# Optimization experiments

Measured on AMD Instinct MI355X. Metric: run time of the kernel, lower is better.

## Reference

```python
import jax, jax.numpy as jnp
import numpy as np

N = 50000      # nodes
E = 800000     # edges (before self-loops)
H = 4          # heads
C = 64         # hidden_unit per head
IN = 256       # input_dim
OUT = 64       # output_dim
NEG = 0.2      # LeakyReLU slope in GATConv
EPS = 1e-5     # BatchNorm eps


def setup_inputs() -> dict:
    key = jax.random.key(0)
    ks = jax.random.split(key, 12)
    s = 0.05
    HC = H * C
    return {
        'x': jax.random.normal(ks[0], (N, IN), dtype=jnp.float32),
        'edge_index': jax.random.randint(ks[1], (2, E), 0, N, dtype=jnp.int64),
        # GATConv layer 1
        'W1': jax.random.normal(ks[2], (IN, HC), dtype=jnp.float32) * s,
        'att_src1': jax.random.normal(ks[3], (H, C), dtype=jnp.float32) * s,
        'att_dst1': jax.random.normal(ks[4], (H, C), dtype=jnp.float32) * s,
        'b1': jnp.zeros((HC,), jnp.float32),
        # GATConv layer 2
        'W2': jax.random.normal(ks[5], (HC, HC), dtype=jnp.float32) * s,
        'att_src2': jax.random.normal(ks[6], (H, C), dtype=jnp.float32) * s,
        'att_dst2': jax.random.normal(ks[7], (H, C), dtype=jnp.float32) * s,
        'b2': jnp.zeros((HC,), jnp.float32),
        # BatchNorms
        'g1': jnp.ones((HC,), jnp.float32), 'beta1': jnp.zeros((HC,), jnp.float32),
        'g2': jnp.ones((HC,), jnp.float32), 'beta2': jnp.zeros((HC,), jnp.float32),
        # final Linear
        'Wl': jax.random.normal(ks[8], (HC, OUT), dtype=jnp.float32) * s,
        'bl': jnp.zeros((OUT,), jnp.float32),
    }


def gat_layer(x, src, dst, W, a_src, a_dst, b):
    # x: [N, F_in] -> per-head features [N, H, C]
    xh = (x @ W).reshape(-1, H, C)
    alpha_src = jnp.einsum('nhc,hc->nh', xh, a_src)   # [N, H]
    alpha_dst = jnp.einsum('nhc,hc->nh', xh, a_dst)   # [N, H]
    e = jax.nn.leaky_relu(alpha_src[src] + alpha_dst[dst], NEG)  # [Etot, H]
    # segment softmax over edges grouped by destination node
    m = jax.ops.segment_max(e, dst, num_segments=N)              # [N, H]
    ex = jnp.exp(e - m[dst])
    den = jax.ops.segment_sum(ex, dst, num_segments=N)           # [N, H]
    alpha = ex / (den[dst] + 1e-16)                              # [Etot, H]
    # weighted scatter-add aggregation
    out = jax.ops.segment_sum(alpha[:, :, None] * xh[src], dst, num_segments=N)
    return out.reshape(-1, H * C) + b


def batchnorm(x, g, beta):
    mu = x.mean(axis=0)
    var = x.var(axis=0)
    return (x - mu) * jax.lax.rsqrt(var + EPS) * g + beta


def reference(x, edge_index, W1, att_src1, att_dst1, b1,
              W2, att_src2, att_dst2, b2, g1, beta1, g2, beta2, Wl, bl):
    # GATConv adds self-loops by default
    loops = jnp.arange(N, dtype=edge_index.dtype)
    src = jnp.concatenate([edge_index[0], loops])
    dst = jnp.concatenate([edge_index[1], loops])
    h = batchnorm(gat_layer(x, src, dst, W1, att_src1, att_dst1, b1), g1, beta1)
    # dropout is identity in eval mode
    h = batchnorm(gat_layer(h, src, dst, W2, att_src2, att_dst2, b2), g2, beta2)
    emb = h @ Wl + bl
    out = jax.nn.log_softmax(emb, axis=1)
    return (out, emb)
```

## Files before the change

### kernel.cpp

```cpp
#include <hip/hip_runtime.h>
#include <cstdint>

#define NNODES 50000
#define NEDGES 800000
#define ETOT   (NEDGES + NNODES)
#define HEADS 4
#define CH 64
#define HC 256
#define INDIM 256
#define OUTDIM 64
#define NEG_SLOPE 0.2f
#define BN_EPS 1e-5f
#define NB 128

typedef unsigned short u16;
typedef __attribute__((ext_vector_type(8))) short short8;
typedef __attribute__((ext_vector_type(8))) unsigned short ushort8v;
typedef __attribute__((ext_vector_type(4))) float floatx4;

__device__ inline float bf2f(u16 u) {
    union { unsigned int i; float f; } c;
    c.i = ((unsigned int)u) << 16;
    return c.f;
}
__device__ inline u16 f2bf(float f) {
    union { float f; unsigned int i; } c;
    c.f = f;
    unsigned int u = c.i + 0x7fff + ((c.i >> 16) & 1);
    return (u16)(u >> 16);
}
__device__ inline void async16(u16* lds, const u16* g) {
    __builtin_amdgcn_global_load_lds(
        (const __attribute__((address_space(1))) unsigned int*)g,
        (__attribute__((address_space(3))) unsigned int*)lds,
        16, 0, 0);
}


__global__ void hist_kernel(const int* __restrict__ ei, int* __restrict__ cnt) {
    int t = blockIdx.x * blockDim.x + threadIdx.x;
    if (t >= ETOT) return;
    int d = (t < NEDGES) ? ei[NEDGES + t] : (t - NEDGES);
    atomicAdd(&cnt[d], 1);
}

__global__ void scan1_kernel(const int* __restrict__ cnt, int* __restrict__ row_off,
                             int* __restrict__ blockSums) {
    __shared__ int tsum[256];
    const int tid = threadIdx.x;
    const int base = blockIdx.x * 4096 + tid * 16;
    int local[16];
    int run = 0;
#pragma unroll
    for (int i = 0; i < 16; ++i) {
        int idx = base + i;
        int v = (idx < NNODES) ? cnt[idx] : 0;
        local[i] = run;
        run += v;
    }
    tsum[tid] = run;
    __syncthreads();
    for (int d = 1; d < 256; d <<= 1) {
        int v = (tid >= d) ? tsum[tid - d] : 0;
        __syncthreads();
        tsum[tid] += v;
        __syncthreads();
    }
    int excl = (tid == 0) ? 0 : tsum[tid - 1];
#pragma unroll
    for (int i = 0; i < 16; ++i) {
        int idx = base + i;
        if (idx < NNODES) row_off[idx] = excl + local[i];
    }
    if (tid == 0) blockSums[blockIdx.x] = tsum[255];
}

__global__ void scan2_kernel(int* __restrict__ row_off, const int* __restrict__ blockSums,
                             int* __restrict__ nxt) {
    __shared__ int sprefix;
    if (threadIdx.x == 0) {
        int p = 0;
        for (int b = 0; b < (int)blockIdx.x; ++b) p += blockSums[b];
        sprefix = p;
    }
    __syncthreads();
    int prefix = sprefix;
    int base = blockIdx.x * 4096 + threadIdx.x * 16;
#pragma unroll
    for (int i = 0; i < 16; ++i) {
        int idx = base + i;
        if (idx < NNODES) {
            int v = row_off[idx] + prefix;
            row_off[idx] = v;
            nxt[idx] = v;
        }
    }
    if (blockIdx.x == 0 && threadIdx.x == 0) row_off[NNODES] = ETOT;
}

__global__ void fill_csr_kernel(const int* __restrict__ ei, int* __restrict__ nxt,
                                int* __restrict__ csr_src, int* __restrict__ csr_dst) {
    int t = blockIdx.x * blockDim.x + threadIdx.x;
    if (t >= ETOT) return;
    int s, d;
    if (t < NEDGES) { s = ei[t]; d = ei[NEDGES + t]; }
    else            { s = d = t - NEDGES; }
    int pos = atomicAdd(&nxt[d], 1);
    csr_src[pos] = s;
    csr_dst[pos] = d;
}


__global__ void castx_kernel(const float* __restrict__ x, u16* __restrict__ xb, int n4) {
    int t = blockIdx.x * blockDim.x + threadIdx.x;
    if (t >= n4) return;
    float4 v = *(const float4*)&x[(size_t)t * 4];
    ushort4 o;
    o.x = f2bf(v.x); o.y = f2bf(v.y); o.z = f2bf(v.z); o.w = f2bf(v.w);
    *(ushort4*)&xb[(size_t)t * 4] = o;
}

__global__ void wcast_kernel(const float* __restrict__ W, u16* __restrict__ Wt,
                             int K, int Ncols) {
    int t = blockIdx.x * blockDim.x + threadIdx.x;
    if (t >= K * Ncols) return;
    int k = t / Ncols, n = t - k * Ncols;
    Wt[n * K + k] = f2bf(W[t]);
}


__global__ __launch_bounds__(256)
void gemm_bf16_kernel(const u16* __restrict__ A, const u16* __restrict__ Bt,
                      u16* __restrict__ Cbf, const float* __restrict__ bias,
                      int M, int Ncols, int K) {
    __shared__ u16 As[128 * 32];
    __shared__ u16 Bs[128 * 32];
    const int tid = threadIdx.x;
    const int wave = tid >> 6, lane = tid & 63;
    const int q15 = lane & 15, quad = lane >> 4;
    const int rowBase = blockIdx.y * 128;
    const int colBase = blockIdx.x * 128;
    const int waveM = (wave >> 1) * 64, waveN = (wave & 1) * 64;

    floatx4 acc[4][4];
    floatx4 zero = {0.f, 0.f, 0.f, 0.f};
#pragma unroll
    for (int i = 0; i < 4; ++i)
#pragma unroll
        for (int j = 0; j < 4; ++j) acc[i][j] = zero;

    for (int kt = 0; kt < K; kt += 32) {
#pragma unroll
        for (int q = 0; q < 2; ++q) {
            int e8 = (wave * 2 + q) * 64 + lane;
            int r = e8 >> 2;
            int c = (e8 & 3) * 8;
            int ar = rowBase + r; if (ar >= M) ar = M - 1;
            async16(&As[(wave * 2 + q) * 512], &A[(size_t)ar * K + kt + c]);
            int br = colBase + r; if (br >= Ncols) br = Ncols - 1;
            async16(&Bs[(wave * 2 + q) * 512], &Bt[(size_t)br * K + kt + c]);
        }
        __syncthreads();

        short8 af[4], bfr[4];
#pragma unroll
        for (int i = 0; i < 4; ++i)
            af[i] = *(const short8*)&As[(waveM + i * 16 + q15) * 32 + quad * 8];
#pragma unroll
        for (int j = 0; j < 4; ++j)
            bfr[j] = *(const short8*)&Bs[(waveN + j * 16 + q15) * 32 + quad * 8];
#pragma unroll
        for (int i = 0; i < 4; ++i)
#pragma unroll
            for (int j = 0; j < 4; ++j)
                acc[i][j] = __builtin_amdgcn_mfma_f32_16x16x32_bf16(af[i], bfr[j], acc[i][j], 0, 0, 0);
        __syncthreads();
    }

#pragma unroll
    for (int i = 0; i < 4; ++i) {
#pragma unroll
        for (int j = 0; j < 4; ++j) {
            int gcol = colBase + waveN + j * 16 + q15;
            if (gcol >= Ncols) continue;
            float bv = bias ? bias[gcol] : 0.f;
#pragma unroll
            for (int r = 0; r < 4; ++r) {
                int grow = rowBase + waveM + i * 16 + quad * 4 + r;
                if (grow >= M) continue;
                Cbf[(size_t)grow * Ncols + gcol] = f2bf(acc[i][j][r] + bv);
            }
        }
    }
}


__global__ void alpha_kernel(const u16* __restrict__ xh,
                             const float* __restrict__ att_src,
                             const float* __restrict__ att_dst,
                             float* __restrict__ as_, float* __restrict__ ad_) {
    int t = blockIdx.x * blockDim.x + threadIdx.x;
    if (t >= NNODES * HEADS) return;
    int n = t >> 2, h = t & 3;
    const u16* xp = xh + (size_t)n * HC + h * CH;
    const float* sp = att_src + h * CH;
    const float* dp = att_dst + h * CH;
    float s = 0.f, d = 0.f;
#pragma unroll
    for (int c = 0; c < CH; c += 8) {
        ushort8v xv = *(const ushort8v*)&xp[c];
#pragma unroll
        for (int i = 0; i < 8; ++i) {
            float v = bf2f(xv[i]);
            s += v * sp[c + i];
            d += v * dp[c + i];
        }
    }
    as_[t] = s;
    ad_[t] = d;
}


__global__ void wedge_kernel(const int* __restrict__ csr_src, const int* __restrict__ csr_dst,
                             const float* __restrict__ asrc, const float* __restrict__ adst,
                             float* __restrict__ w4) {
    int e = blockIdx.x * blockDim.x + threadIdx.x;
    if (e >= ETOT) return;
    int s = csr_src[e], d = csr_dst[e];
    float4 a = *(const float4*)&asrc[s * 4];
    float4 b = *(const float4*)&adst[d * 4];
    float4 r;
    float v;
    v = a.x + b.x; v = v > 0.f ? v : NEG_SLOPE * v; r.x = __expf(v);
    v = a.y + b.y; v = v > 0.f ? v : NEG_SLOPE * v; r.y = __expf(v);
    v = a.z + b.z; v = v > 0.f ? v : NEG_SLOPE * v; r.z = __expf(v);
    v = a.w + b.w; v = v > 0.f ? v : NEG_SLOPE * v; r.w = __expf(v);
    *(float4*)&w4[(size_t)e * 4] = r;
}


__global__ __launch_bounds__(256)
void aggregate_kernel(const int* __restrict__ row_off, const int* __restrict__ csr_src,
                      const float* __restrict__ w4, const u16* __restrict__ xh,
                      const float* __restrict__ bias, u16* __restrict__ out) {
    const int g = threadIdx.x >> 6;
    const int lane = threadIdx.x & 63;
    const int d = blockIdx.x * 4 + g;
    const int h = lane >> 4;
    const int cbase = lane * 4;
    const int start = row_off[d], end = row_off[d + 1];
    float a0 = 0.f, a1 = 0.f, a2 = 0.f, a3 = 0.f, den = 0.f;
    int e = start;
    for (; e + 3 < end; e += 4) {
        int s0 = csr_src[e], s1 = csr_src[e + 1], s2 = csr_src[e + 2], s3 = csr_src[e + 3];
        float w0 = w4[(size_t)e * 4 + h];
        float w1 = w4[(size_t)(e + 1) * 4 + h];
        float w2 = w4[(size_t)(e + 2) * 4 + h];
        float w3 = w4[(size_t)(e + 3) * 4 + h];
        ushort4 x0 = *(const ushort4*)&xh[(size_t)s0 * HC + cbase];
        ushort4 x1 = *(const ushort4*)&xh[(size_t)s1 * HC + cbase];
        ushort4 x2 = *(const ushort4*)&xh[(size_t)s2 * HC + cbase];
        ushort4 x3 = *(const ushort4*)&xh[(size_t)s3 * HC + cbase];
        den += (w0 + w1) + (w2 + w3);
        a0 += w0 * bf2f(x0.x) + w1 * bf2f(x1.x) + w2 * bf2f(x2.x) + w3 * bf2f(x3.x);
        a1 += w0 * bf2f(x0.y) + w1 * bf2f(x1.y) + w2 * bf2f(x2.y) + w3 * bf2f(x3.y);
        a2 += w0 * bf2f(x0.z) + w1 * bf2f(x1.z) + w2 * bf2f(x2.z) + w3 * bf2f(x3.z);
        a3 += w0 * bf2f(x0.w) + w1 * bf2f(x1.w) + w2 * bf2f(x2.w) + w3 * bf2f(x3.w);
    }
    for (; e < end; ++e) {
        int s0 = csr_src[e];
        float w0 = w4[(size_t)e * 4 + h];
        ushort4 x0 = *(const ushort4*)&xh[(size_t)s0 * HC + cbase];
        den += w0;
        a0 += w0 * bf2f(x0.x);
        a1 += w0 * bf2f(x0.y);
        a2 += w0 * bf2f(x0.z);
        a3 += w0 * bf2f(x0.w);
    }
    float inv = 1.f / (den + 1e-16f);
    ushort4 o;
    o.x = f2bf(a0 * inv + bias[cbase + 0]);
    o.y = f2bf(a1 * inv + bias[cbase + 1]);
    o.z = f2bf(a2 * inv + bias[cbase + 2]);
    o.w = f2bf(a3 * inv + bias[cbase + 3]);
    *(ushort4*)&out[(size_t)d * HC + cbase] = o;
}


__global__ __launch_bounds__(256)
void bn_stats_kernel(const u16* __restrict__ x, float* __restrict__ part) {
    const int tid = threadIdx.x;
    float s[8] = {}, s2[8] = {};
    const size_t total = (size_t)NNODES * HC;
    const size_t stride = (size_t)NB * 256 * 8;
    for (size_t f = ((size_t)blockIdx.x * 256 + tid) * 8; f < total; f += stride) {
        ushort8v v = *(const ushort8v*)&x[f];
#pragma unroll
        for (int i = 0; i < 8; ++i) {
            float t = bf2f(v[i]);
            s[i] += t;
            s2[i] += t * t;
        }
    }
#pragma unroll
    for (int i = 0; i < 8; ++i) {
        s[i] += __shfl_xor(s[i], 32, 64);
        s2[i] += __shfl_xor(s2[i], 32, 64);
    }
    __shared__ float red[4][512];
    const int wave = tid >> 6, lane = tid & 63;
    if (lane < 32) {
#pragma unroll
        for (int i = 0; i < 8; ++i) {
            red[wave][lane * 8 + i] = s[i];
            red[wave][256 + lane * 8 + i] = s2[i];
        }
    }
    __syncthreads();
    for (int j = tid; j < 512; j += 256)
        part[(size_t)blockIdx.x * 512 + j] = red[0][j] + red[1][j] + red[2][j] + red[3][j];
}


__global__ __launch_bounds__(256)
void fold_kernel(const float* __restrict__ W, const float* __restrict__ part,
                 const float* __restrict__ g, const float* __restrict__ beta,
                 const float* __restrict__ baseBias,
                 u16* __restrict__ Wt, float* __restrict__ biasOut, int Ncols) {
    __shared__ float sh[256];
    __shared__ float stat2[2];
    const int b = blockIdx.x;
    const int tid = threadIdx.x;
    if (b < 256) {
        const int wave = tid >> 6, lane = tid & 63;
        if (wave < 2) {
            int off = wave * 256;
            float v = part[(size_t)lane * 512 + off + b] + part[(size_t)(lane + 64) * 512 + off + b];
#pragma unroll
            for (int o = 1; o <= 32; o <<= 1) v += __shfl_xor(v, o, 64);
            if (lane == 0) stat2[wave] = v;
        }
        __syncthreads();
        float mu = stat2[0] * (1.f / NNODES);
        float var = stat2[1] * (1.f / NNODES) - mu * mu;
        float rg = rsqrtf(var + BN_EPS) * g[b];
        for (int n = tid; n < Ncols; n += 256)
            Wt[n * 256 + b] = f2bf(W[b * Ncols + n] * rg);
    } else {
        float sum = 0.f, sq = 0.f;
        for (int k = 0; k < NB; ++k) {
            sum += part[(size_t)k * 512 + tid];
            sq += part[(size_t)k * 512 + 256 + tid];
        }
        float mu = sum * (1.f / NNODES);
        float var = sq * (1.f / NNODES) - mu * mu;
        float rg = rsqrtf(var + BN_EPS) * g[tid];
        sh[tid] = beta[tid] - mu * rg;
        __syncthreads();
        if (tid < Ncols) {
            float acc = baseBias ? baseBias[tid] : 0.f;
            for (int k = 0; k < 256; ++k) acc += sh[k] * W[k * Ncols + tid];
            biasOut[tid] = acc;
        }
    }
}


__global__ __launch_bounds__(256)
void final_ls_kernel(const u16* __restrict__ A, const u16* __restrict__ Bt,
                     const float* __restrict__ bias,
                     float* __restrict__ emb, float* __restrict__ out, int M) {
    __shared__ u16 As[256 * 32];
    __shared__ u16 Bs[64 * 32];
    const int tid = threadIdx.x;
    const int wave = tid >> 6, lane = tid & 63;
    const int q15 = lane & 15, quad = lane >> 4;
    const int rowBase = blockIdx.x * 256;

    floatx4 acc[4][4];
    floatx4 zero = {0.f, 0.f, 0.f, 0.f};
#pragma unroll
    for (int i = 0; i < 4; ++i)
#pragma unroll
        for (int j = 0; j < 4; ++j) acc[i][j] = zero;

    for (int kt = 0; kt < 256; kt += 32) {
#pragma unroll
        for (int rnd = 0; rnd < 4; ++rnd) {
            int slot = rnd * 256 + wave * 64 + lane;
            int r = slot >> 2;
            int c = (slot & 3) * 8;
            int ar = rowBase + r; if (ar >= M) ar = M - 1;
            async16(&As[(rnd * 256 + wave * 64) * 8], &A[(size_t)ar * 256 + kt + c]);
        }
        {
            int slot = wave * 64 + lane;
            int r = slot >> 2;
            int c = (slot & 3) * 8;
            async16(&Bs[(wave * 64) * 8], &Bt[(size_t)r * 256 + kt + c]);
        }
        __syncthreads();

        short8 af[4], bfr[4];
#pragma unroll
        for (int i = 0; i < 4; ++i)
            af[i] = *(const short8*)&As[(wave * 64 + i * 16 + q15) * 32 + quad * 8];
#pragma unroll
        for (int j = 0; j < 4; ++j)
            bfr[j] = *(const short8*)&Bs[(j * 16 + q15) * 32 + quad * 8];
#pragma unroll
        for (int i = 0; i < 4; ++i)
#pragma unroll
            for (int j = 0; j < 4; ++j)
                acc[i][j] = __builtin_amdgcn_mfma_f32_16x16x32_bf16(af[i], bfr[j], acc[i][j], 0, 0, 0);
        __syncthreads();
    }

#pragma unroll
    for (int i = 0; i < 4; ++i) {
#pragma unroll
        for (int rr = 0; rr < 4; ++rr) {
            float v[4];
#pragma unroll
            for (int j = 0; j < 4; ++j) v[j] = acc[i][j][rr] + bias[j * 16 + q15];
            float m = fmaxf(fmaxf(v[0], v[1]), fmaxf(v[2], v[3]));
#pragma unroll
            for (int off = 1; off <= 8; off <<= 1) m = fmaxf(m, __shfl_xor(m, off, 64));
            float s = __expf(v[0] - m) + __expf(v[1] - m) + __expf(v[2] - m) + __expf(v[3] - m);
#pragma unroll
            for (int off = 1; off <= 8; off <<= 1) s += __shfl_xor(s, off, 64);
            float ls = m + logf(s);
            int grow = rowBase + wave * 64 + i * 16 + quad * 4 + rr;
            if (grow < M) {
#pragma unroll
                for (int j = 0; j < 4; ++j) {
                    int col = j * 16 + q15;
                    emb[(size_t)grow * OUTDIM + col] = v[j];
                    out[(size_t)grow * OUTDIM + col] = v[j] - ls;
                }
            }
        }
    }
}


extern "C" void kernel_launch(void* const* d_in, const int* in_sizes, int n_in,
                              void* d_out, int out_size, void* d_ws, size_t ws_size,
                              hipStream_t stream) {
    const float* x   = (const float*)d_in[0];
    const int*   ei  = (const int*)d_in[1];
    const float* W1  = (const float*)d_in[2];
    const float* at_s1 = (const float*)d_in[3];
    const float* at_d1 = (const float*)d_in[4];
    const float* b1  = (const float*)d_in[5];
    const float* W2  = (const float*)d_in[6];
    const float* at_s2 = (const float*)d_in[7];
    const float* at_d2 = (const float*)d_in[8];
    const float* b2  = (const float*)d_in[9];
    const float* g1  = (const float*)d_in[10];
    const float* be1 = (const float*)d_in[11];
    const float* g2  = (const float*)d_in[12];
    const float* be2 = (const float*)d_in[13];
    const float* Wl  = (const float*)d_in[14];
    const float* bl  = (const float*)d_in[15];

    float* out = (float*)d_out;
    float* emb = out + (size_t)NNODES * OUTDIM;

    char* ws = (char*)d_ws;
    size_t off = 0;
    auto alloc = [&](size_t bytes) {
        void* p = ws + off;
        off += (bytes + 255) & ~(size_t)255;
        return p;
    };
    int*   cnt     = (int*)alloc((size_t)NNODES * 4);
    int*   row_off = (int*)alloc((size_t)(NNODES + 1) * 4);
    int*   nxt     = (int*)alloc((size_t)NNODES * 4);
    int*   bsums   = (int*)alloc(64 * 4);
    int*   csr_src = (int*)alloc((size_t)ETOT * 4);
    int*   csr_dst = (int*)alloc((size_t)ETOT * 4);
    float* w4      = (float*)alloc((size_t)ETOT * 4 * 4);
    float* asrc    = (float*)alloc((size_t)NNODES * 4 * 4);
    float* adst    = (float*)alloc((size_t)NNODES * 4 * 4);
    u16*   x_bf    = (u16*)alloc((size_t)NNODES * HC * 2);
    u16*   xh_bf   = (u16*)alloc((size_t)NNODES * HC * 2);
    u16*   ag_bf   = (u16*)alloc((size_t)NNODES * HC * 2);
    u16*   w1t     = (u16*)alloc((size_t)HC * INDIM * 2);
    u16*   w2t     = (u16*)alloc((size_t)HC * HC * 2);
    u16*   wlt     = (u16*)alloc((size_t)OUTDIM * HC * 2);
    float* part    = (float*)alloc((size_t)NB * 512 * 4);
    float* bias2   = (float*)alloc(HC * 4);
    float* blp     = (float*)alloc(OUTDIM * 4);

    const int scanBlocks = (NNODES + 4095) / 4096;
    const int eBlocks = (ETOT + 255) / 256;

    hipMemsetAsync(cnt, 0, (size_t)NNODES * 4, stream);
    hist_kernel<<<eBlocks, 256, 0, stream>>>(ei, cnt);
    scan1_kernel<<<scanBlocks, 256, 0, stream>>>(cnt, row_off, bsums);
    scan2_kernel<<<scanBlocks, 256, 0, stream>>>(row_off, bsums, nxt);
    fill_csr_kernel<<<eBlocks, 256, 0, stream>>>(ei, nxt, csr_src, csr_dst);

    castx_kernel<<<(NNODES * HC / 4 + 255) / 256, 256, 0, stream>>>(x, x_bf, NNODES * HC / 4);
    wcast_kernel<<<(INDIM * HC + 255) / 256, 256, 0, stream>>>(W1, w1t, INDIM, HC);

    dim3 gemmGrid(2, (NNODES + 127) / 128);
    int nhBlocks = (NNODES * HEADS + 255) / 256;

    gemm_bf16_kernel<<<gemmGrid, 256, 0, stream>>>(x_bf, w1t, xh_bf, nullptr, NNODES, HC, INDIM);
    alpha_kernel<<<nhBlocks, 256, 0, stream>>>(xh_bf, at_s1, at_d1, asrc, adst);
    wedge_kernel<<<eBlocks, 256, 0, stream>>>(csr_src, csr_dst, asrc, adst, w4);
    aggregate_kernel<<<NNODES / 4, 256, 0, stream>>>(row_off, csr_src, w4, xh_bf, b1, ag_bf);
    bn_stats_kernel<<<NB, 256, 0, stream>>>(ag_bf, part);
    fold_kernel<<<257, 256, 0, stream>>>(W2, part, g1, be1, nullptr, w2t, bias2, HC);

    gemm_bf16_kernel<<<gemmGrid, 256, 0, stream>>>(ag_bf, w2t, xh_bf, bias2, NNODES, HC, HC);
    alpha_kernel<<<nhBlocks, 256, 0, stream>>>(xh_bf, at_s2, at_d2, asrc, adst);
    wedge_kernel<<<eBlocks, 256, 0, stream>>>(csr_src, csr_dst, asrc, adst, w4);
    aggregate_kernel<<<NNODES / 4, 256, 0, stream>>>(row_off, csr_src, w4, xh_bf, b2, ag_bf);
    bn_stats_kernel<<<NB, 256, 0, stream>>>(ag_bf, part);
    fold_kernel<<<257, 256, 0, stream>>>(Wl, part, g2, be2, bl, wlt, blp, OUTDIM);

    final_ls_kernel<<<(NNODES + 255) / 256, 256, 0, stream>>>(ag_bf, wlt, blp, emb, out, NNODES);
}
```

Before: 557.5 us.

## Fuse input cast and attention logits into GEMM, permute xh layout, store edge weights in bf16

The first GEMM now reads fp32 x directly and converts it to bf16 while staging it into LDS, which removes the separate cast kernel and its round trip through memory. Both GEMMs compute the per-head attention dot products in the epilogue with lane shuffles, so the alpha kernel is gone. The GEMM output is written in a permuted per-head layout so each lane stores ushort4 packs, and the aggregate kernel reads that layout and writes scattered u16 outputs. Edge weights are stored as bf16 to halve their traffic, and the aggregate loop is unrolled by 8 for more loads in flight. This costs some exp-weight precision and the synchronous fp32 A load in the first GEMM.

```diff
diff --git a/kernel.cpp b/kernel.cpp
--- a/kernel.cpp
+++ b/kernel.cpp
@@ -14,6 +14,7 @@
 #define NB 128
 
 typedef unsigned short u16;
+typedef unsigned int u32;
 typedef __attribute__((ext_vector_type(8))) short short8;
 typedef __attribute__((ext_vector_type(8))) unsigned short ushort8v;
 typedef __attribute__((ext_vector_type(4))) float floatx4;
@@ -111,15 +112,6 @@
 }
 
 
-__global__ void castx_kernel(const float* __restrict__ x, u16* __restrict__ xb, int n4) {
-    int t = blockIdx.x * blockDim.x + threadIdx.x;
-    if (t >= n4) return;
-    float4 v = *(const float4*)&x[(size_t)t * 4];
-    ushort4 o;
-    o.x = f2bf(v.x); o.y = f2bf(v.y); o.z = f2bf(v.z); o.w = f2bf(v.w);
-    *(ushort4*)&xb[(size_t)t * 4] = o;
-}
-
 __global__ void wcast_kernel(const float* __restrict__ W, u16* __restrict__ Wt,
                              int K, int Ncols) {
     int t = blockIdx.x * blockDim.x + threadIdx.x;
@@ -129,10 +121,13 @@
 }
 
 
+template <bool AF32>
 __global__ __launch_bounds__(256)
-void gemm_bf16_kernel(const u16* __restrict__ A, const u16* __restrict__ Bt,
-                      u16* __restrict__ Cbf, const float* __restrict__ bias,
-                      int M, int Ncols, int K) {
+void gemm_gat_kernel(const void* __restrict__ Ap, const u16* __restrict__ Bt,
+                     const float* __restrict__ bias,
+                     const float* __restrict__ att_s, const float* __restrict__ att_d,
+                     u16* __restrict__ xhp, float* __restrict__ asrc,
+                     float* __restrict__ adst, int M, int K) {
     __shared__ u16 As[128 * 32];
     __shared__ u16 Bs[128 * 32];
     const int tid = threadIdx.x;
@@ -141,6 +136,7 @@
     const int rowBase = blockIdx.y * 128;
     const int colBase = blockIdx.x * 128;
     const int waveM = (wave >> 1) * 64, waveN = (wave & 1) * 64;
+    const int head = blockIdx.x * 2 + (wave & 1);
 
     floatx4 acc[4][4];
     floatx4 zero = {0.f, 0.f, 0.f, 0.f};
@@ -150,15 +146,34 @@
         for (int j = 0; j < 4; ++j) acc[i][j] = zero;
 
     for (int kt = 0; kt < K; kt += 32) {
-#pragma unroll
-        for (int q = 0; q < 2; ++q) {
-            int e8 = (wave * 2 + q) * 64 + lane;
-            int r = e8 >> 2;
-            int c = (e8 & 3) * 8;
-            int ar = rowBase + r; if (ar >= M) ar = M - 1;
-            async16(&As[(wave * 2 + q) * 512], &A[(size_t)ar * K + kt + c]);
-            int br = colBase + r; if (br >= Ncols) br = Ncols - 1;
-            async16(&Bs[(wave * 2 + q) * 512], &Bt[(size_t)br * K + kt + c]);
+        if constexpr (AF32) {
+            const float* A32 = (const float*)Ap;
+#pragma unroll
+            for (int rnd = 0; rnd < 4; ++rnd) {
+                int slot = rnd * 256 + tid;
+                int r = slot >> 3, c4 = (slot & 7) * 4;
+                int ar = rowBase + r; if (ar >= M) ar = M - 1;
+                float4 fv = *(const float4*)&A32[(size_t)ar * K + kt + c4];
+                ushort4 o;
+                o.x = f2bf(fv.x); o.y = f2bf(fv.y); o.z = f2bf(fv.z); o.w = f2bf(fv.w);
+                *(ushort4*)&As[r * 32 + c4] = o;
+            }
+#pragma unroll
+            for (int q = 0; q < 2; ++q) {
+                int e8 = (wave * 2 + q) * 64 + lane;
+                int r = e8 >> 2, c = (e8 & 3) * 8;
+                async16(&Bs[(wave * 2 + q) * 512], &Bt[(size_t)(colBase + r) * K + kt + c]);
+            }
+        } else {
+            const u16* A16 = (const u16*)Ap;
+#pragma unroll
+            for (int q = 0; q < 2; ++q) {
+                int e8 = (wave * 2 + q) * 64 + lane;
+                int r = e8 >> 2, c = (e8 & 3) * 8;
+                int ar = rowBase + r; if (ar >= M) ar = M - 1;
+                async16(&As[(wave * 2 + q) * 512], &A16[(size_t)ar * K + kt + c]);
+                async16(&Bs[(wave * 2 + q) * 512], &Bt[(size_t)(colBase + r) * K + kt + c]);
+            }
         }
         __syncthreads();
 
@@ -177,113 +192,113 @@
         __syncthreads();
     }
 
+    float bv[4], atsv[4], atdv[4];
+#pragma unroll
+    for (int j = 0; j < 4; ++j) {
+        int gcol = colBase + waveN + j * 16 + q15;
+        bv[j] = bias ? bias[gcol] : 0.f;
+        int hc = head * CH + j * 16 + q15;
+        atsv[j] = att_s[hc];
+        atdv[j] = att_d[hc];
+    }
+    const int pbase = head * 64 + q15 * 4;
+
 #pragma unroll
     for (int i = 0; i < 4; ++i) {
 #pragma unroll
-        for (int j = 0; j < 4; ++j) {
-            int gcol = colBase + waveN + j * 16 + q15;
-            if (gcol >= Ncols) continue;
-            float bv = bias ? bias[gcol] : 0.f;
-#pragma unroll
-            for (int r = 0; r < 4; ++r) {
-                int grow = rowBase + waveM + i * 16 + quad * 4 + r;
-                if (grow >= M) continue;
-                Cbf[(size_t)grow * Ncols + gcol] = f2bf(acc[i][j][r] + bv);
+        for (int rr = 0; rr < 4; ++rr) {
+            int grow = rowBase + waveM + i * 16 + quad * 4 + rr;
+            float v[4];
+#pragma unroll
+            for (int j = 0; j < 4; ++j) v[j] = acc[i][j][rr] + bv[j];
+            float s = v[0] * atsv[0] + v[1] * atsv[1] + v[2] * atsv[2] + v[3] * atsv[3];
+            float d = v[0] * atdv[0] + v[1] * atdv[1] + v[2] * atdv[2] + v[3] * atdv[3];
+#pragma unroll
+            for (int off = 1; off <= 8; off <<= 1) {
+                s += __shfl_xor(s, off, 64);
+                d += __shfl_xor(d, off, 64);
             }
-        }
-    }
-}
-
-
-__global__ void alpha_kernel(const u16* __restrict__ xh,
-                             const float* __restrict__ att_src,
-                             const float* __restrict__ att_dst,
-                             float* __restrict__ as_, float* __restrict__ ad_) {
-    int t = blockIdx.x * blockDim.x + threadIdx.x;
-    if (t >= NNODES * HEADS) return;
-    int n = t >> 2, h = t & 3;
-    const u16* xp = xh + (size_t)n * HC + h * CH;
-    const float* sp = att_src + h * CH;
-    const float* dp = att_dst + h * CH;
-    float s = 0.f, d = 0.f;
-#pragma unroll
-    for (int c = 0; c < CH; c += 8) {
-        ushort8v xv = *(const ushort8v*)&xp[c];
-#pragma unroll
-        for (int i = 0; i < 8; ++i) {
-            float v = bf2f(xv[i]);
-            s += v * sp[c + i];
-            d += v * dp[c + i];
-        }
-    }
-    as_[t] = s;
-    ad_[t] = d;
+            ushort4 o;
+            o.x = f2bf(v[0]); o.y = f2bf(v[1]); o.z = f2bf(v[2]); o.w = f2bf(v[3]);
+            if (grow < M) {
+                *(ushort4*)&xhp[(size_t)grow * HC + pbase] = o;
+                if (q15 == 0) {
+                    asrc[grow * 4 + head] = s;
+                    adst[grow * 4 + head] = d;
+                }
+            }
+        }
+    }
 }
 
 
 __global__ void wedge_kernel(const int* __restrict__ csr_src, const int* __restrict__ csr_dst,
                              const float* __restrict__ asrc, const float* __restrict__ adst,
-                             float* __restrict__ w4) {
+                             u16* __restrict__ w4b) {
     int e = blockIdx.x * blockDim.x + threadIdx.x;
     if (e >= ETOT) return;
     int s = csr_src[e], d = csr_dst[e];
     float4 a = *(const float4*)&asrc[s * 4];
     float4 b = *(const float4*)&adst[d * 4];
-    float4 r;
+    ushort4 r;
     float v;
-    v = a.x + b.x; v = v > 0.f ? v : NEG_SLOPE * v; r.x = __expf(v);
-    v = a.y + b.y; v = v > 0.f ? v : NEG_SLOPE * v; r.y = __expf(v);
-    v = a.z + b.z; v = v > 0.f ? v : NEG_SLOPE * v; r.z = __expf(v);
-    v = a.w + b.w; v = v > 0.f ? v : NEG_SLOPE * v; r.w = __expf(v);
-    *(float4*)&w4[(size_t)e * 4] = r;
+    v = a.x + b.x; v = v > 0.f ? v : NEG_SLOPE * v; r.x = f2bf(__expf(v));
+    v = a.y + b.y; v = v > 0.f ? v : NEG_SLOPE * v; r.y = f2bf(__expf(v));
+    v = a.z + b.z; v = v > 0.f ? v : NEG_SLOPE * v; r.z = f2bf(__expf(v));
+    v = a.w + b.w; v = v > 0.f ? v : NEG_SLOPE * v; r.w = f2bf(__expf(v));
+    *(ushort4*)&w4b[(size_t)e * 4] = r;
 }
 
 
 __global__ __launch_bounds__(256)
 void aggregate_kernel(const int* __restrict__ row_off, const int* __restrict__ csr_src,
-                      const float* __restrict__ w4, const u16* __restrict__ xh,
+                      const u16* __restrict__ w4b, const u16* __restrict__ xhp,
                       const float* __restrict__ bias, u16* __restrict__ out) {
     const int g = threadIdx.x >> 6;
     const int lane = threadIdx.x & 63;
     const int d = blockIdx.x * 4 + g;
     const int h = lane >> 4;
-    const int cbase = lane * 4;
+    const int c16 = lane & 15;
+    const int poff = h * 64 + c16 * 4;
     const int start = row_off[d], end = row_off[d + 1];
     float a0 = 0.f, a1 = 0.f, a2 = 0.f, a3 = 0.f, den = 0.f;
     int e = start;
-    for (; e + 3 < end; e += 4) {
-        int s0 = csr_src[e], s1 = csr_src[e + 1], s2 = csr_src[e + 2], s3 = csr_src[e + 3];
-        float w0 = w4[(size_t)e * 4 + h];
-        float w1 = w4[(size_t)(e + 1) * 4 + h];
-        float w2 = w4[(size_t)(e + 2) * 4 + h];
-        float w3 = w4[(size_t)(e + 3) * 4 + h];
-        ushort4 x0 = *(const ushort4*)&xh[(size_t)s0 * HC + cbase];
-        ushort4 x1 = *(const ushort4*)&xh[(size_t)s1 * HC + cbase];
-        ushort4 x2 = *(const ushort4*)&xh[(size_t)s2 * HC + cbase];
-        ushort4 x3 = *(const ushort4*)&xh[(size_t)s3 * HC + cbase];
-        den += (w0 + w1) + (w2 + w3);
-        a0 += w0 * bf2f(x0.x) + w1 * bf2f(x1.x) + w2 * bf2f(x2.x) + w3 * bf2f(x3.x);
-        a1 += w0 * bf2f(x0.y) + w1 * bf2f(x1.y) + w2 * bf2f(x2.y) + w3 * bf2f(x3.y);
-        a2 += w0 * bf2f(x0.z) + w1 * bf2f(x1.z) + w2 * bf2f(x2.z) + w3 * bf2f(x3.z);
-        a3 += w0 * bf2f(x0.w) + w1 * bf2f(x1.w) + w2 * bf2f(x2.w) + w3 * bf2f(x3.w);
+    for (; e + 7 < end; e += 8) {
+        int sidx[8];
+        u16 wv[8];
+        ushort4 xv[8];
+#pragma unroll
+        for (int k = 0; k < 8; ++k) sidx[k] = csr_src[e + k];
+#pragma unroll
+        for (int k = 0; k < 8; ++k) wv[k] = w4b[(size_t)(e + k) * 4 + h];
+#pragma unroll
+        for (int k = 0; k < 8; ++k) xv[k] = *(const ushort4*)&xhp[(size_t)sidx[k] * HC + poff];
+#pragma unroll
+        for (int k = 0; k < 8; ++k) {
+            float w = bf2f(wv[k]);
+            den += w;
+            a0 += w * bf2f(xv[k].x);
+            a1 += w * bf2f(xv[k].y);
+            a2 += w * bf2f(xv[k].z);
+            a3 += w * bf2f(xv[k].w);
+        }
     }
     for (; e < end; ++e) {
         int s0 = csr_src[e];
-        float w0 = w4[(size_t)e * 4 + h];
-        ushort4 x0 = *(const ushort4*)&xh[(size_t)s0 * HC + cbase];
-        den += w0;
-        a0 += w0 * bf2f(x0.x);
-        a1 += w0 * bf2f(x0.y);
-        a2 += w0 * bf2f(x0.z);
-        a3 += w0 * bf2f(x0.w);
+        float w = bf2f(w4b[(size_t)e * 4 + h]);
+        ushort4 x0 = *(const ushort4*)&xhp[(size_t)s0 * HC + poff];
+        den += w;
+        a0 += w * bf2f(x0.x);
+        a1 += w * bf2f(x0.y);
+        a2 += w * bf2f(x0.z);
+        a3 += w * bf2f(x0.w);
     }
     float inv = 1.f / (den + 1e-16f);
-    ushort4 o;
-    o.x = f2bf(a0 * inv + bias[cbase + 0]);
-    o.y = f2bf(a1 * inv + bias[cbase + 1]);
-    o.z = f2bf(a2 * inv + bias[cbase + 2]);
-    o.w = f2bf(a3 * inv + bias[cbase + 3]);
-    *(ushort4*)&out[(size_t)d * HC + cbase] = o;
+    const int ch0 = h * 64 + c16;
+    out[(size_t)d * HC + ch0 +  0] = f2bf(a0 * inv + bias[ch0 +  0]);
+    out[(size_t)d * HC + ch0 + 16] = f2bf(a1 * inv + bias[ch0 + 16]);
+    out[(size_t)d * HC + ch0 + 32] = f2bf(a2 * inv + bias[ch0 + 32]);
+    out[(size_t)d * HC + ch0 + 48] = f2bf(a3 * inv + bias[ch0 + 48]);
 }
 
 
@@ -480,11 +495,10 @@
     int*   bsums   = (int*)alloc(64 * 4);
     int*   csr_src = (int*)alloc((size_t)ETOT * 4);
     int*   csr_dst = (int*)alloc((size_t)ETOT * 4);
-    float* w4      = (float*)alloc((size_t)ETOT * 4 * 4);
+    u16*   w4b     = (u16*)alloc((size_t)ETOT * 4 * 2);
     float* asrc    = (float*)alloc((size_t)NNODES * 4 * 4);
     float* adst    = (float*)alloc((size_t)NNODES * 4 * 4);
-    u16*   x_bf    = (u16*)alloc((size_t)NNODES * HC * 2);
-    u16*   xh_bf   = (u16*)alloc((size_t)NNODES * HC * 2);
+    u16*   xhp     = (u16*)alloc((size_t)NNODES * HC * 2);
     u16*   ag_bf   = (u16*)alloc((size_t)NNODES * HC * 2);
     u16*   w1t     = (u16*)alloc((size_t)HC * INDIM * 2);
     u16*   w2t     = (u16*)alloc((size_t)HC * HC * 2);
@@ -502,23 +516,21 @@
     scan2_kernel<<<scanBlocks, 256, 0, stream>>>(row_off, bsums, nxt);
     fill_csr_kernel<<<eBlocks, 256, 0, stream>>>(ei, nxt, csr_src, csr_dst);
 
-    castx_kernel<<<(NNODES * HC / 4 + 255) / 256, 256, 0, stream>>>(x, x_bf, NNODES * HC / 4);
     wcast_kernel<<<(INDIM * HC + 255) / 256, 256, 0, stream>>>(W1, w1t, INDIM, HC);
 
     dim3 gemmGrid(2, (NNODES + 127) / 128);
-    int nhBlocks = (NNODES * HEADS + 255) / 256;
-
-    gemm_bf16_kernel<<<gemmGrid, 256, 0, stream>>>(x_bf, w1t, xh_bf, nullptr, NNODES, HC, INDIM);
-    alpha_kernel<<<nhBlocks, 256, 0, stream>>>(xh_bf, at_s1, at_d1, asrc, adst);
-    wedge_kernel<<<eBlocks, 256, 0, stream>>>(csr_src, csr_dst, asrc, adst, w4);
-    aggregate_kernel<<<NNODES / 4, 256, 0, stream>>>(row_off, csr_src, w4, xh_bf, b1, ag_bf);
+
+    gemm_gat_kernel<true><<<gemmGrid, 256, 0, stream>>>(x, w1t, nullptr, at_s1, at_d1,
+                                                        xhp, asrc, adst, NNODES, INDIM);
+    wedge_kernel<<<eBlocks, 256, 0, stream>>>(csr_src, csr_dst, asrc, adst, w4b);
+    aggregate_kernel<<<NNODES / 4, 256, 0, stream>>>(row_off, csr_src, w4b, xhp, b1, ag_bf);
     bn_stats_kernel<<<NB, 256, 0, stream>>>(ag_bf, part);
     fold_kernel<<<257, 256, 0, stream>>>(W2, part, g1, be1, nullptr, w2t, bias2, HC);
 
-    gemm_bf16_kernel<<<gemmGrid, 256, 0, stream>>>(ag_bf, w2t, xh_bf, bias2, NNODES, HC, HC);
-    alpha_kernel<<<nhBlocks, 256, 0, stream>>>(xh_bf, at_s2, at_d2, asrc, adst);
-    wedge_kernel<<<eBlocks, 256, 0, stream>>>(csr_src, csr_dst, asrc, adst, w4);
-    aggregate_kernel<<<NNODES / 4, 256, 0, stream>>>(row_off, csr_src, w4, xh_bf, b2, ag_bf);
+    gemm_gat_kernel<false><<<gemmGrid, 256, 0, stream>>>(ag_bf, w2t, bias2, at_s2, at_d2,
+                                                         xhp, asrc, adst, NNODES, HC);
+    wedge_kernel<<<eBlocks, 256, 0, stream>>>(csr_src, csr_dst, asrc, adst, w4b);
+    aggregate_kernel<<<NNODES / 4, 256, 0, stream>>>(row_off, csr_src, w4b, xhp, b2, ag_bf);
     bn_stats_kernel<<<NB, 256, 0, stream>>>(ag_bf, part);
     fold_kernel<<<257, 256, 0, stream>>>(Wl, part, g2, be2, bl, wlt, blp, OUTDIM);
 
```

New measurement: 503.1 us. -9.8%, faster.
